# Kernel optimization log

Hardware: AMD Instinct MI355X
Metric: run time of the kernel (lower is better)

Reference implementation:

```python
import jax, jax.numpy as jnp
import numpy as np

EPS = 1e-5


def farthest_point_sample(points, npoint):
    # points: [B, N, 3]; returns idx [B, npoint] (int32)
    B, N, _ = points.shape
    # is_center=True: start from the point farthest from the centroid
    centroid = points.mean(axis=1, keepdims=True)            # [B,1,3]
    d0 = jnp.sum((points - centroid) ** 2, axis=-1)           # [B,N]
    farthest = jnp.argmax(d0, axis=-1)                        # [B]
    distance = jnp.full((B, N), 1e10, dtype=points.dtype)

    def step(carry, _):
        dist, far = carry
        cent = jnp.take_along_axis(points, far[:, None, None], axis=1)  # [B,1,3]
        d = jnp.sum((points - cent) ** 2, axis=-1)                       # [B,N]
        dist = jnp.minimum(dist, d)
        new_far = jnp.argmax(dist, axis=-1)
        return (dist, new_far), far

    (_, _), idx = jax.lax.scan(step, (distance, farthest), None, length=npoint)
    return idx.T  # [B, npoint]


def index_points(x, idx):
    # x: [B, N, C], idx: [B, S] -> [B, S, C]
    return jnp.take_along_axis(x, idx[:, :, None], axis=1)


def setup_inputs() -> dict:
    key = jax.random.key(0)
    k1, k2, k3, k4 = jax.random.split(key, 4)
    B, N, in_dim, out_dim = 8, 16384, 128, 256
    points = jax.random.normal(k1, (B, N, 3), dtype=jnp.float32)
    features = jax.random.normal(k2, (B, N, in_dim), dtype=jnp.float32)
    W = jax.random.normal(k3, (out_dim, in_dim), dtype=jnp.float32) * (1.0 / np.sqrt(in_dim))
    b = jax.random.normal(k4, (out_dim,), dtype=jnp.float32) * 0.01
    return {"points": points, "features": features, "W": W, "b": b, "num_points": 4096}


def reference(points, features, W, b, num_points):
    # conv1x1 on features.transpose(-1,-2): [B,in,N] -> [B,out,N]
    x = jnp.einsum('bnc,oc->bon', features, W) + b[None, :, None]  # [B,out,N]
    # InstanceNorm1d (affine=False): normalize over spatial dim N per (b, channel)
    mu = x.mean(axis=-1, keepdims=True)
    var = x.var(axis=-1, keepdims=True)
    x = (x - mu) * jax.lax.rsqrt(var + EPS)
    x = jax.nn.relu(x)
    feats = x.transpose(0, 2, 1)  # [B,N,out]

    idx = farthest_point_sample(points, num_points)  # [B, num_points]
    sampled_points = index_points(points, idx)
    sampled_features = index_points(feats, idx)
    return sampled_points, sampled_features
```

## Files before the change

### kernel.cpp

```cpp
#include <hip/hip_runtime.h>
#include <math.h>

#define B_      8
#define N_      16384
#define CIN_    128
#define COUT_   256
#define NS_     4096

typedef unsigned long long u64;

static __device__ __forceinline__ float sqdist_xla(float px, float py, float pz,
                                                   float cx, float cy, float cz) {
  float dx = __fsub_rn(px, cx);
  float dy = __fsub_rn(py, cy);
  float dz = __fsub_rn(pz, cz);
  return __fmaf_rn(dz, dz, __fmaf_rn(dy, dy, __fmul_rn(dx, dx)));
}

static __device__ __forceinline__ float wave64_max_dpp(float x) {
  int v = __float_as_int(x);
  #define DPPSTEP(ctrl, rm, bm) { \
    const int t = __builtin_amdgcn_update_dpp(0, v, (ctrl), (rm), (bm), false); \
    v = __float_as_int(fmaxf(__int_as_float(v), __int_as_float(t))); }
  DPPSTEP(0x111, 0xf, 0xf)
  DPPSTEP(0x112, 0xf, 0xf)
  DPPSTEP(0x114, 0xf, 0xe)
  DPPSTEP(0x118, 0xf, 0xc)
  DPPSTEP(0x142, 0xa, 0xf)
  DPPSTEP(0x143, 0xc, 0xf)
  #undef DPPSTEP
  return __int_as_float(v);
}

__global__ __launch_bounds__(1024) void k1_fps_gram(
    const float* __restrict__ points, const float* __restrict__ features,
    float* __restrict__ outP, int* __restrict__ idxw,
    float* __restrict__ Gred, float* __restrict__ Sred)
{
  __shared__ __align__(16) char LDSB[131072 + 128];
  const int tid = threadIdx.x;

  if (blockIdx.x < B_) {
    const int b = blockIdx.x;
    const float* __restrict__ P = points + (size_t)b * N_ * 3;
    float2*   __restrict__ sXY   = (float2*)LDSB;
    u64*      __restrict__ cellI = (u64*)(LDSB + 131072);
    unsigned* __restrict__ cellV = (unsigned*)(LDSB + 131072 + 16);
    float*    __restrict__ cent  = (float*)(LDSB + 131072 + 24);
    const int lane = tid & 63;

    float z_[16];
    #pragma unroll
    for (int k = 0; k < 16; ++k) {
      const int n = k * 1024 + tid;
      sXY[n] = make_float2(P[3*n+0], P[3*n+1]);
      z_[k]  = P[3*n+2];
    }
    #pragma unroll
    for (int k = 0; k < 16; ++k) asm volatile("" : "+v"(z_[k]));

    if (tid < 3) {
      const int c = tid;
      float acc = P[c];
      for (int n = 1; n < N_; ++n) acc = __fadd_rn(acc, P[3*n + c]);
      cent[c] = __fmul_rn(acc, 6.103515625e-05f);
    }
    if (tid == 0) {
      cellI[0] = ~0ULL; cellI[1] = ~0ULL;
      cellV[0] = 0u;    cellV[1] = 0u;
    }
    __syncthreads();

    float dd[16];
    float ccx, ccy, ccz;

    {
      const float cx0 = cent[0], cy0 = cent[1], cz0 = cent[2];
      float tlm = -1.0f;
      #pragma unroll
      for (int k = 0; k < 16; ++k) {
        const int n = k * 1024 + tid;
        const float2 xy = sXY[n];
        const float d = sqdist_xla(xy.x, xy.y, z_[k], cx0, cy0, cz0);
        dd[k] = d;
        tlm = fmaxf(tlm, d);
      }
      const float wlm = wave64_max_dpp(tlm);
      if (lane == 63) atomicMax(&cellV[0], (unsigned)__float_as_int(wlm));
      __syncthreads();
      const float bv = __int_as_float((int)cellV[0]);
      if (tid == 0) { cellV[1] = 0u; cellI[1] = ~0ULL; }
      if (tlm == bv) {
        int kb = 0x7FFFFFFF;
        #pragma unroll
        for (int k = 15; k >= 0; --k) kb = (dd[k] == bv) ? k : kb;
        float zz = z_[0];
        #pragma unroll
        for (int k = 1; k < 16; ++k) zz = (kb == k) ? z_[k] : zz;
        const u64 key = ((u64)(unsigned)(kb * 1024 + tid) << 32)
                      | (u64)(unsigned)__float_as_int(zz);
        atomicMin(&cellI[0], key);
      }
      __syncthreads();
      const u64 cw = cellI[0];
      const int far = (int)(cw >> 32);
      ccz = __int_as_float((int)(unsigned)cw);
      const float2 xy = sXY[far];
      ccx = xy.x; ccy = xy.y;
      if (tid == 0) {
        const size_t ob = (size_t)b * NS_;
        outP[ob*3+0] = ccx; outP[ob*3+1] = ccy; outP[ob*3+2] = ccz;
        idxw[ob] = far;
      }
    }
    #pragma unroll
    for (int k = 0; k < 16; ++k) dd[k] = 1e10f;

    for (int s = 1; s < NS_; ++s) {
      const int par = s & 1;
      float tlm = -1.0f;
      #pragma unroll
      for (int k = 0; k < 16; ++k) {
        const int n = k * 1024 + tid;
        const float2 xy = sXY[n];
        const float d  = sqdist_xla(xy.x, xy.y, z_[k], ccx, ccy, ccz);
        const float nd = fminf(dd[k], d);
        dd[k] = nd;
        tlm = fmaxf(tlm, nd);
      }
      const float wlm = wave64_max_dpp(tlm);
      if (lane == 63) atomicMax(&cellV[par], (unsigned)__float_as_int(wlm));
      __syncthreads();
      const float bv = __int_as_float((int)cellV[par]);
      if (tid == 0) { cellV[par ^ 1] = 0u; cellI[par ^ 1] = ~0ULL; }
      if (tlm == bv) {
        int kb = 0x7FFFFFFF;
        #pragma unroll
        for (int k = 15; k >= 0; --k) kb = (dd[k] == bv) ? k : kb;
        float zz = z_[0];
        #pragma unroll
        for (int k = 1; k < 16; ++k) zz = (kb == k) ? z_[k] : zz;
        const u64 key = ((u64)(unsigned)(kb * 1024 + tid) << 32)
                      | (u64)(unsigned)__float_as_int(zz);
        atomicMin(&cellI[par], key);
      }
      __syncthreads();
      const u64 cw = cellI[par];
      const int far = (int)(cw >> 32);
      ccz = __int_as_float((int)(unsigned)cw);
      const float2 xy = sXY[far];
      ccx = xy.x; ccy = xy.y;
      if (tid == 0) {
        const size_t ob = (size_t)b * NS_ + s;
        outP[ob*3+0] = ccx; outP[ob*3+1] = ccy; outP[ob*3+2] = ccz;
        idxw[ob] = far;
      }
    }
  } else {
    float* __restrict__ Lf = (float*)LDSB;
    const int b = (int)blockIdx.x - B_;
    float acc[4][4];
    #pragma unroll
    for (int i = 0; i < 4; ++i)
      #pragma unroll
      for (int j = 0; j < 4; ++j) acc[i][j] = 0.f;
    float sacc = 0.f;
    const int ti = tid >> 5;
    const int tj = tid & 31;
    const float* fb = features + (size_t)b * N_ * CIN_;
    for (int t32 = 0; t32 < N_/32; ++t32) {
      const float4 v0 = *(const float4*)(fb + ((size_t)t32 * 32 + ti) * CIN_ + tj * 4);
      __syncthreads();
      *(float4*)&Lf[ti*128 + tj*4] = v0;
      __syncthreads();
      #pragma unroll 4
      for (int r = 0; r < 32; ++r) {
        const float4 a4 = *(const float4*)&Lf[r*128 + ti*4];
        const float4 b4 = *(const float4*)&Lf[r*128 + tj*4];
        const float av[4] = {a4.x, a4.y, a4.z, a4.w};
        const float bw[4] = {b4.x, b4.y, b4.z, b4.w};
        #pragma unroll
        for (int i = 0; i < 4; ++i)
          #pragma unroll
          for (int j = 0; j < 4; ++j) acc[i][j] = fmaf(av[i], bw[j], acc[i][j]);
      }
      if (tid < 128) {
        #pragma unroll 8
        for (int r = 0; r < 32; ++r) sacc += Lf[r*128 + tid];
      }
    }
    float* gp = Gred + (size_t)b * (CIN_*CIN_);
    #pragma unroll
    for (int i = 0; i < 4; ++i)
      #pragma unroll
      for (int j = 0; j < 4; ++j)
        gp[(ti*4+i)*CIN_ + tj*4 + j] = acc[i][j];
    if (tid < 128) Sred[b*CIN_ + tid] = sacc;
  }
}

__global__ __launch_bounds__(128) void k2b_stats(
    const float* __restrict__ Gred, const float* __restrict__ Sred,
    const float* __restrict__ W, const float* __restrict__ bias,
    float* __restrict__ stats)
{
  const int b = blockIdx.x >> 8;
  const int o = blockIdx.x & 255;
  const int tid = threadIdx.x;
  __shared__ float sw[CIN_];
  __shared__ float r1[CIN_], r2[CIN_];
  sw[tid] = W[(size_t)o*CIN_ + tid];
  __syncthreads();
  const float* gr = Gred + (size_t)b*CIN_*CIN_ + (size_t)tid*CIN_;
  float g = 0.f;
  #pragma unroll 8
  for (int j = 0; j < CIN_; ++j) g = fmaf(gr[j], sw[j], g);
  r1[tid] = g * sw[tid];
  r2[tid] = sw[tid] * Sred[b*CIN_ + tid];
  __syncthreads();
  for (int stp = 64; stp > 0; stp >>= 1) {
    if (tid < stp) { r1[tid] += r1[tid+stp]; r2[tid] += r2[tid+stp]; }
    __syncthreads();
  }
  if (tid == 0) {
    const float wGw = r1[0], wS = r2[0], bo = bias[o];
    const float invN = 1.0f / (float)N_;
    const float mu  = wS*invN + bo;
    const float ex2 = (wGw + 2.0f*bo*wS)*invN + bo*bo;
    float var = ex2 - mu*mu;
    var = fmaxf(var, 0.0f);
    const float sc = 1.0f / sqrtf(var + 1e-5f);
    stats[((size_t)(b*COUT_ + o))*2 + 0] = wS*invN;
    stats[((size_t)(b*COUT_ + o))*2 + 1] = sc;
  }
}

__global__ __launch_bounds__(256) void k3_out(
    const float* __restrict__ features, const float* __restrict__ W,
    const int* __restrict__ idxw, const float* __restrict__ stats,
    float* __restrict__ outF)
{
  const int tid = threadIdx.x;
  const int b  = blockIdx.x >> 8;
  const int r  = blockIdx.x & 255;
  const int st = r >> 2, ot = r & 3;
  const int s0 = st * 64, o0 = ot * 64;

  __shared__ float Fs[64][129];
  __shared__ float Wt[64][129];
  __shared__ int   sIdx[64];
  __shared__ float sSub[64], sSc[64];

  if (tid < 64) sIdx[tid] = idxw[b*NS_ + s0 + tid];
  if (tid >= 64 && tid < 128) {
    const int oo = tid - 64;
    sSub[oo] = stats[((size_t)(b*COUT_ + o0 + oo))*2 + 0];
    sSc[oo]  = stats[((size_t)(b*COUT_ + o0 + oo))*2 + 1];
  }
  __syncthreads();
  {
    const int row = tid >> 2;
    const int q   = tid & 3;
    const float* fsrc = features + ((size_t)b*N_ + sIdx[row]) * CIN_;
    const float* wsrc = W + (size_t)(o0 + row) * CIN_;
    #pragma unroll
    for (int v = 0; v < 8; ++v) {
      const int c = q*4 + v*16;
      const float4 fv = *(const float4*)(fsrc + c);
      const float4 wv = *(const float4*)(wsrc + c);
      Fs[row][c+0]=fv.x; Fs[row][c+1]=fv.y; Fs[row][c+2]=fv.z; Fs[row][c+3]=fv.w;
      Wt[row][c+0]=wv.x; Wt[row][c+1]=wv.y; Wt[row][c+2]=wv.z; Wt[row][c+3]=wv.w;
    }
  }
  __syncthreads();

  const int ts = tid >> 4, to = tid & 15;
  float acc[4][4];
  #pragma unroll
  for (int i = 0; i < 4; ++i)
    #pragma unroll
    for (int j = 0; j < 4; ++j) acc[i][j] = 0.f;

  #pragma unroll 4
  for (int k = 0; k < CIN_; ++k) {
    const float a0 = Fs[ts*4+0][k], a1 = Fs[ts*4+1][k], a2 = Fs[ts*4+2][k], a3 = Fs[ts*4+3][k];
    const float w0 = Wt[to*4+0][k], w1 = Wt[to*4+1][k], w2 = Wt[to*4+2][k], w3 = Wt[to*4+3][k];
    acc[0][0]=fmaf(a0,w0,acc[0][0]); acc[0][1]=fmaf(a0,w1,acc[0][1]); acc[0][2]=fmaf(a0,w2,acc[0][2]); acc[0][3]=fmaf(a0,w3,acc[0][3]);
    acc[1][0]=fmaf(a1,w0,acc[1][0]); acc[1][1]=fmaf(a1,w1,acc[1][1]); acc[1][2]=fmaf(a1,w2,acc[1][2]); acc[1][3]=fmaf(a1,w3,acc[1][3]);
    acc[2][0]=fmaf(a2,w0,acc[2][0]); acc[2][1]=fmaf(a2,w1,acc[2][1]); acc[2][2]=fmaf(a2,w2,acc[2][2]); acc[2][3]=fmaf(a2,w3,acc[2][3]);
    acc[3][0]=fmaf(a3,w0,acc[3][0]); acc[3][1]=fmaf(a3,w1,acc[3][1]); acc[3][2]=fmaf(a3,w2,acc[3][2]); acc[3][3]=fmaf(a3,w3,acc[3][3]);
  }

  #pragma unroll
  for (int i = 0; i < 4; ++i) {
    float4 o4;
    o4.x = fmaxf((acc[i][0] - sSub[to*4+0]) * sSc[to*4+0], 0.f);
    o4.y = fmaxf((acc[i][1] - sSub[to*4+1]) * sSc[to*4+1], 0.f);
    o4.z = fmaxf((acc[i][2] - sSub[to*4+2]) * sSc[to*4+2], 0.f);
    o4.w = fmaxf((acc[i][3] - sSub[to*4+3]) * sSc[to*4+3], 0.f);
    *(float4*)&outF[((size_t)b*NS_ + s0 + ts*4 + i)*COUT_ + o0 + to*4] = o4;
  }
}

extern "C" void kernel_launch(void* const* d_in, const int* in_sizes, int n_in,
                              void* d_out, int out_size, void* d_ws, size_t ws_size,
                              hipStream_t stream) {
  (void)in_sizes; (void)n_in; (void)out_size; (void)ws_size;
  const float* points   = (const float*)d_in[0];
  const float* features = (const float*)d_in[1];
  const float* W        = (const float*)d_in[2];
  const float* bias     = (const float*)d_in[3];
  float* out  = (float*)d_out;
  float* outP = out;
  float* outF = out + (size_t)B_*NS_*3;

  char* ws = (char*)d_ws;
  int*   idxw  = (int*)  (ws + 0);
  float* Gred  = (float*)(ws + 131072);
  float* Sred  = (float*)(ws + 655360);
  float* stats = (float*)(ws + 659456);

  k1_fps_gram<<<dim3(B_ + B_),  dim3(1024), 0, stream>>>(points, features, outP, idxw, Gred, Sred);
  k2b_stats  <<<dim3(B_*COUT_), dim3(CIN_), 0, stream>>>(Gred, Sred, W, bias, stats);
  k3_out     <<<dim3(B_*256),   dim3(256),  0, stream>>>(features, W, idxw, stats, outF);
}
```

Measured before the change: 5.915 ms.

## Fuse FPS argmax into single packed atomic with one barrier per step

New measurement: 6.404 ms. 8.3% more time.

```diff
diff --git a/kernel.cpp b/kernel.cpp
--- a/kernel.cpp
+++ b/kernel.cpp
@@ -17,7 +17,7 @@
   return __fmaf_rn(dz, dz, __fmaf_rn(dy, dy, __fmul_rn(dx, dx)));
 }
 
-static __device__ __forceinline__ float wave64_max_dpp(float x) {
+static __device__ __forceinline__ float wave64_max_bcast(float x) {
   int v = __float_as_int(x);
   #define DPPSTEP(ctrl, rm, bm) { \
     const int t = __builtin_amdgcn_update_dpp(0, v, (ctrl), (rm), (bm), false); \
@@ -29,7 +29,7 @@
   DPPSTEP(0x142, 0xa, 0xf)
   DPPSTEP(0x143, 0xc, 0xf)
   #undef DPPSTEP
-  return __int_as_float(v);
+  return __int_as_float(__builtin_amdgcn_readlane(v, 63));
 }
 
 __global__ __launch_bounds__(1024) void k1_fps_gram(
@@ -43,10 +43,9 @@
   if (blockIdx.x < B_) {
     const int b = blockIdx.x;
     const float* __restrict__ P = points + (size_t)b * N_ * 3;
-    float2*   __restrict__ sXY   = (float2*)LDSB;
-    u64*      __restrict__ cellI = (u64*)(LDSB + 131072);
-    unsigned* __restrict__ cellV = (unsigned*)(LDSB + 131072 + 16);
-    float*    __restrict__ cent  = (float*)(LDSB + 131072 + 24);
+    float2* __restrict__ sXY  = (float2*)LDSB;
+    u64*    __restrict__ cell = (u64*)(LDSB + 131072);
+    float*  __restrict__ cent = (float*)(LDSB + 131072 + 32);
     const int lane = tid & 63;
 
     float z_[16];
@@ -65,14 +64,12 @@
       for (int n = 1; n < N_; ++n) acc = __fadd_rn(acc, P[3*n + c]);
       cent[c] = __fmul_rn(acc, 6.103515625e-05f);
     }
-    if (tid == 0) {
-      cellI[0] = ~0ULL; cellI[1] = ~0ULL;
-      cellV[0] = 0u;    cellV[1] = 0u;
-    }
+    if (tid == 0) { cell[0] = ~0ULL; cell[1] = ~0ULL; cell[2] = ~0ULL; }
     __syncthreads();
 
     float dd[16];
-    float ccx, ccy, ccz;
+    float ccx, ccy, zc;
+    int far;
 
     {
       const float cx0 = cent[0], cy0 = cent[1], cz0 = cent[2];
@@ -85,31 +82,24 @@
         dd[k] = d;
         tlm = fmaxf(tlm, d);
       }
-      const float wlm = wave64_max_dpp(tlm);
-      if (lane == 63) atomicMax(&cellV[0], (unsigned)__float_as_int(wlm));
+      const float wvm = wave64_max_bcast(tlm);
+      if (tlm == wvm) {
+        int kb = 0;
+        #pragma unroll
+        for (int k = 15; k >= 0; --k) kb = (dd[k] == tlm) ? k : kb;
+        const unsigned n = (unsigned)(kb * 1024 + tid);
+        const u64 key = ((u64)(~(unsigned)__float_as_int(tlm)) << 32) | (u64)n;
+        atomicMin(&cell[0], key);
+      }
       __syncthreads();
-      const float bv = __int_as_float((int)cellV[0]);
-      if (tid == 0) { cellV[1] = 0u; cellI[1] = ~0ULL; }
-      if (tlm == bv) {
-        int kb = 0x7FFFFFFF;
-        #pragma unroll
-        for (int k = 15; k >= 0; --k) kb = (dd[k] == bv) ? k : kb;
-        float zz = z_[0];
-        #pragma unroll
-        for (int k = 1; k < 16; ++k) zz = (kb == k) ? z_[k] : zz;
-        const u64 key = ((u64)(unsigned)(kb * 1024 + tid) << 32)
-                      | (u64)(unsigned)__float_as_int(zz);
-        atomicMin(&cellI[0], key);
-      }
-      __syncthreads();
-      const u64 cw = cellI[0];
-      const int far = (int)(cw >> 32);
-      ccz = __int_as_float((int)(unsigned)cw);
+      const u64 cw = cell[0];
+      far = (int)(unsigned)cw;
       const float2 xy = sXY[far];
       ccx = xy.x; ccy = xy.y;
+      zc  = P[3*(size_t)far + 2];
       if (tid == 0) {
         const size_t ob = (size_t)b * NS_;
-        outP[ob*3+0] = ccx; outP[ob*3+1] = ccy; outP[ob*3+2] = ccz;
+        outP[ob*3+0] = ccx; outP[ob*3+1] = ccy; outP[ob*3+2] = zc;
         idxw[ob] = far;
       }
     }
@@ -117,42 +107,53 @@
     for (int k = 0; k < 16; ++k) dd[k] = 1e10f;
 
     for (int s = 1; s < NS_; ++s) {
-      const int par = s & 1;
+      const int par = s % 3;
+      const int rst = (s + 1) % 3;
+      float t[8];
+      #pragma unroll
+      for (int k = 0; k < 8; ++k) {
+        const float2 xy = sXY[k * 1024 + tid];
+        const float dx = __fsub_rn(xy.x, ccx);
+        const float dy = __fsub_rn(xy.y, ccy);
+        t[k] = __fmaf_rn(dy, dy, __fmul_rn(dx, dx));
+      }
+      if (tid == 0) cell[rst] = ~0ULL;
+      const float ccz = zc;
       float tlm = -1.0f;
       #pragma unroll
-      for (int k = 0; k < 16; ++k) {
-        const int n = k * 1024 + tid;
-        const float2 xy = sXY[n];
+      for (int k = 0; k < 8; ++k) {
+        const float dz = __fsub_rn(z_[k], ccz);
+        const float d  = __fmaf_rn(dz, dz, t[k]);
+        const float nd = fminf(dd[k], d);
+        dd[k] = nd;
+        tlm = fmaxf(tlm, nd);
+      }
+      #pragma unroll
+      for (int k = 8; k < 16; ++k) {
+        const float2 xy = sXY[k * 1024 + tid];
         const float d  = sqdist_xla(xy.x, xy.y, z_[k], ccx, ccy, ccz);
         const float nd = fminf(dd[k], d);
         dd[k] = nd;
         tlm = fmaxf(tlm, nd);
       }
-      const float wlm = wave64_max_dpp(tlm);
-      if (lane == 63) atomicMax(&cellV[par], (unsigned)__float_as_int(wlm));
+      const float wvm = wave64_max_bcast(tlm);
+      if (tlm == wvm) {
+        int kb = 0;
+        #pragma unroll
+        for (int k = 15; k >= 0; --k) kb = (dd[k] == tlm) ? k : kb;
+        const unsigned n = (unsigned)(kb * 1024 + tid);
+        const u64 key = ((u64)(~(unsigned)__float_as_int(tlm)) << 32) | (u64)n;
+        atomicMin(&cell[par], key);
+      }
       __syncthreads();
-      const float bv = __int_as_float((int)cellV[par]);
-      if (tid == 0) { cellV[par ^ 1] = 0u; cellI[par ^ 1] = ~0ULL; }
-      if (tlm == bv) {
-        int kb = 0x7FFFFFFF;
-        #pragma unroll
-        for (int k = 15; k >= 0; --k) kb = (dd[k] == bv) ? k : kb;
-        float zz = z_[0];
-        #pragma unroll
-        for (int k = 1; k < 16; ++k) zz = (kb == k) ? z_[k] : zz;
-        const u64 key = ((u64)(unsigned)(kb * 1024 + tid) << 32)
-                      | (u64)(unsigned)__float_as_int(zz);
-        atomicMin(&cellI[par], key);
-      }
-      __syncthreads();
-      const u64 cw = cellI[par];
-      const int far = (int)(cw >> 32);
-      ccz = __int_as_float((int)(unsigned)cw);
+      const u64 cw = cell[par];
+      far = (int)(unsigned)cw;
       const float2 xy = sXY[far];
       ccx = xy.x; ccy = xy.y;
+      zc  = P[3*(size_t)far + 2];
       if (tid == 0) {
         const size_t ob = (size_t)b * NS_ + s;
-        outP[ob*3+0] = ccx; outP[ob*3+1] = ccy; outP[ob*3+2] = ccz;
+        outP[ob*3+0] = ccx; outP[ob*3+1] = ccy; outP[ob*3+2] = zc;
         idxw[ob] = far;
       }
     }
```

## Pack FPS coordinates pairwise and compute distances with packed f32 instructions

Applied to the files above, without the earlier changes.

Result: slower. 7.414 ms (+25.3%).

```diff
diff --git a/kernel.cpp b/kernel.cpp
--- a/kernel.cpp
+++ b/kernel.cpp
@@ -32,6 +32,13 @@
   return __int_as_float(v);
 }
 
+static __device__ __forceinline__ float2 dbl2f2(double d) {
+  return __builtin_bit_cast(float2, d);
+}
+static __device__ __forceinline__ double f22dbl(float a, float b) {
+  return __builtin_bit_cast(double, make_float2(a, b));
+}
+
 __global__ __launch_bounds__(1024) void k1_fps_gram(
     const float* __restrict__ points, const float* __restrict__ features,
     float* __restrict__ outP, int* __restrict__ idxw,
@@ -43,21 +50,24 @@
   if (blockIdx.x < B_) {
     const int b = blockIdx.x;
     const float* __restrict__ P = points + (size_t)b * N_ * 3;
-    float2*   __restrict__ sXY   = (float2*)LDSB;
+    float2*   __restrict__ sXp   = (float2*)LDSB;
+    float2*   __restrict__ sYp   = (float2*)(LDSB + 65536);
     u64*      __restrict__ cellI = (u64*)(LDSB + 131072);
     unsigned* __restrict__ cellV = (unsigned*)(LDSB + 131072 + 16);
     float*    __restrict__ cent  = (float*)(LDSB + 131072 + 24);
     const int lane = tid & 63;
 
-    float z_[16];
-    #pragma unroll
-    for (int k = 0; k < 16; ++k) {
-      const int n = k * 1024 + tid;
-      sXY[n] = make_float2(P[3*n+0], P[3*n+1]);
-      z_[k]  = P[3*n+2];
-    }
-    #pragma unroll
-    for (int k = 0; k < 16; ++k) asm volatile("" : "+v"(z_[k]));
+    double zp[8];
+    #pragma unroll
+    for (int j = 0; j < 8; ++j) {
+      const int nA = (2*j) * 1024 + tid;
+      const int nB = (2*j+1) * 1024 + tid;
+      sXp[j*1024+tid] = make_float2(P[3*nA+0], P[3*nB+0]);
+      sYp[j*1024+tid] = make_float2(P[3*nA+1], P[3*nB+1]);
+      zp[j] = f22dbl(P[3*nA+2], P[3*nB+2]);
+    }
+    #pragma unroll
+    for (int j = 0; j < 8; ++j) asm volatile("" : "+v"(zp[j]));
 
     if (tid < 3) {
       const int c = tid;
@@ -79,9 +89,14 @@
       float tlm = -1.0f;
       #pragma unroll
       for (int k = 0; k < 16; ++k) {
-        const int n = k * 1024 + tid;
-        const float2 xy = sXY[n];
-        const float d = sqdist_xla(xy.x, xy.y, z_[k], cx0, cy0, cz0);
+        const int j = k >> 1; const bool hi = k & 1;
+        const float2 xp = sXp[j*1024+tid];
+        const float2 yp = sYp[j*1024+tid];
+        const float2 zz = dbl2f2(zp[j]);
+        const float x = hi ? xp.y : xp.x;
+        const float y = hi ? yp.y : yp.x;
+        const float z = hi ? zz.y : zz.x;
+        const float d = sqdist_xla(x, y, z, cx0, cy0, cz0);
         dd[k] = d;
         tlm = fmaxf(tlm, d);
       }
@@ -94,9 +109,12 @@
         int kb = 0x7FFFFFFF;
         #pragma unroll
         for (int k = 15; k >= 0; --k) kb = (dd[k] == bv) ? k : kb;
-        float zz = z_[0];
-        #pragma unroll
-        for (int k = 1; k < 16; ++k) zz = (kb == k) ? z_[k] : zz;
+        float zz = dbl2f2(zp[0]).x;
+        #pragma unroll
+        for (int k = 1; k < 16; ++k) {
+          const float zk = (k & 1) ? dbl2f2(zp[k>>1]).y : dbl2f2(zp[k>>1]).x;
+          zz = (kb == k) ? zk : zz;
+        }
         const u64 key = ((u64)(unsigned)(kb * 1024 + tid) << 32)
                       | (u64)(unsigned)__float_as_int(zz);
         atomicMin(&cellI[0], key);
@@ -105,8 +123,9 @@
       const u64 cw = cellI[0];
       const int far = (int)(cw >> 32);
       ccz = __int_as_float((int)(unsigned)cw);
-      const float2 xy = sXY[far];
-      ccx = xy.x; ccy = xy.y;
+      const int tt = far & 1023, kk = far >> 10, jj = kk >> 1, hh = kk & 1;
+      ccx = ((const float*)sXp)[(jj*1024+tt)*2 + hh];
+      ccy = ((const float*)sYp)[(jj*1024+tt)*2 + hh];
       if (tid == 0) {
         const size_t ob = (size_t)b * NS_;
         outP[ob*3+0] = ccx; outP[ob*3+1] = ccy; outP[ob*3+2] = ccz;
@@ -118,15 +137,25 @@
 
     for (int s = 1; s < NS_; ++s) {
       const int par = s & 1;
+      const double nxx = f22dbl(-ccx, -ccx);
+      const double nyy = f22dbl(-ccy, -ccy);
+      const double nzz = f22dbl(-ccz, -ccz);
       float tlm = -1.0f;
       #pragma unroll
-      for (int k = 0; k < 16; ++k) {
-        const int n = k * 1024 + tid;
-        const float2 xy = sXY[n];
-        const float d  = sqdist_xla(xy.x, xy.y, z_[k], ccx, ccy, ccz);
-        const float nd = fminf(dd[k], d);
-        dd[k] = nd;
-        tlm = fmaxf(tlm, nd);
+      for (int j = 0; j < 8; ++j) {
+        const double xpd = *(const double*)&sXp[j*1024+tid];
+        const double ypd = *(const double*)&sYp[j*1024+tid];
+        double dx, dy, dz, t0, t1, d2;
+        asm("v_pk_add_f32 %0, %1, %2" : "=v"(dx) : "v"(xpd),   "v"(nxx));
+        asm("v_pk_add_f32 %0, %1, %2" : "=v"(dy) : "v"(ypd),   "v"(nyy));
+        asm("v_pk_add_f32 %0, %1, %2" : "=v"(dz) : "v"(zp[j]), "v"(nzz));
+        asm("v_pk_mul_f32 %0, %1, %1" : "=v"(t0) : "v"(dx));
+        asm("v_pk_fma_f32 %0, %1, %1, %2" : "=v"(t1) : "v"(dy), "v"(t0));
+        asm("v_pk_fma_f32 %0, %1, %1, %2" : "=v"(d2) : "v"(dz), "v"(t1));
+        const float2 dp = dbl2f2(d2);
+        const float ndA = fminf(dd[2*j],   dp.x); dd[2*j]   = ndA;
+        const float ndB = fminf(dd[2*j+1], dp.y); dd[2*j+1] = ndB;
+        tlm = fmaxf(tlm, fmaxf(ndA, ndB));
       }
       const float wlm = wave64_max_dpp(tlm);
       if (lane == 63) atomicMax(&cellV[par], (unsigned)__float_as_int(wlm));
@@ -137,9 +166,12 @@
         int kb = 0x7FFFFFFF;
         #pragma unroll
         for (int k = 15; k >= 0; --k) kb = (dd[k] == bv) ? k : kb;
-        float zz = z_[0];
-        #pragma unroll
-        for (int k = 1; k < 16; ++k) zz = (kb == k) ? z_[k] : zz;
+        float zz = dbl2f2(zp[0]).x;
+        #pragma unroll
+        for (int k = 1; k < 16; ++k) {
+          const float zk = (k & 1) ? dbl2f2(zp[k>>1]).y : dbl2f2(zp[k>>1]).x;
+          zz = (kb == k) ? zk : zz;
+        }
         const u64 key = ((u64)(unsigned)(kb * 1024 + tid) << 32)
                       | (u64)(unsigned)__float_as_int(zz);
         atomicMin(&cellI[par], key);
@@ -148,8 +180,9 @@
       const u64 cw = cellI[par];
       const int far = (int)(cw >> 32);
       ccz = __int_as_float((int)(unsigned)cw);
-      const float2 xy = sXY[far];
-      ccx = xy.x; ccy = xy.y;
+      const int tt = far & 1023, kk = far >> 10, jj = kk >> 1, hh = kk & 1;
+      ccx = ((const float*)sXp)[(jj*1024+tt)*2 + hh];
+      ccy = ((const float*)sYp)[(jj*1024+tt)*2 + hh];
       if (tid == 0) {
         const size_t ob = (size_t)b * NS_ + s;
         outP[ob*3+0] = ccx; outP[ob*3+1] = ccy; outP[ob*3+2] = ccz;
```
